# Kernel optimization log

Measured on AMD Instinct MI355X. Metric: run time of the kernel, lower is better.

## Reference

```python
import jax, jax.numpy as jnp
import numpy as np


def setup_inputs() -> dict:
    key = jax.random.key(0)
    k1, k2, k3 = jax.random.split(key, 3)
    B, Cin, H, W = 16, 128, 56, 56
    Cout, Kh, Kw = 256, 3, 3
    tensor = jax.random.normal(k1, (B, Cin, H, W), dtype=jnp.float32)
    weights = jax.random.normal(k2, (Cout, Cin, Kh, Kw), dtype=jnp.float32) * 0.05
    bias = jax.random.normal(k3, (Cout,), dtype=jnp.float32) * 0.05
    return {"tensor": tensor, "weights": weights, "bias": bias}


def reference(tensor, weights, bias):
    # OpticalConvolution: unfold (im2col) -> per-output-channel augmented dot
    # products (w . patch + b). Mathematically this is a standard 2D conv with
    # bias, expressed here as one fused conv instead of a per-channel loop.
    stride, padding, dilation = (1, 1), ((1, 1), (1, 1)), (1, 1)
    out = jax.lax.conv_general_dilated(
        tensor, weights,
        window_strides=stride,
        padding=padding,
        rhs_dilation=dilation,
        dimension_numbers=("NCHW", "OIHW", "NCHW"),
    )
    return out + bias[None, :, None, None]  # [B, Cout, H_out, W_out]
```

## Files before the change

kernel.cpp:

```cpp
#include <hip/hip_runtime.h>

typedef unsigned short ushort_t;
typedef unsigned int uint_t;

#define CIN   128
#define COUT  256
#define HH    56
#define WW    56
#define HWSZ  3136
#define BATCH 16
#define NPIX  50176
#define KTOT  1152

typedef __attribute__((ext_vector_type(8))) short bf16x8;
typedef __attribute__((ext_vector_type(4))) float f32x4;

__device__ __forceinline__ ushort_t f2bf(float v) {
    union { float f; uint_t u; } c; c.f = v;
    uint_t u = c.u;
    u += 0x7FFFu + ((u >> 16) & 1u);
    return (ushort_t)(u >> 16);
}

__global__ void wt_xform(const float* __restrict__ w, ushort_t* __restrict__ out) {
    int idx = blockIdx.x * 256 + threadIdx.x;
    int co  = idx / KTOT;
    int k   = idx - co * KTOT;
    int pos = k >> 7;
    int ci  = k & 127;
    out[idx] = f2bf(w[co * KTOT + ci * 9 + pos]);
}

__global__ void in_xform(const float* __restrict__ in, ushort_t* __restrict__ out) {
    __shared__ ushort_t tile[WW * 130];
    int by = blockIdx.x;
    int b  = by / HH;
    int y  = by - b * HH;
    const float* src = in + (size_t)b * CIN * HWSZ + (size_t)y * WW;
    for (int idx = threadIdx.x; idx < CIN * WW; idx += 256) {
        int ci = idx / WW;
        int x  = idx - ci * WW;
        tile[x * 130 + ci] = f2bf(src[(size_t)ci * HWSZ + x]);
    }
    __syncthreads();
    ushort_t* dst = out + (size_t)by * WW * CIN;
    for (int idx = threadIdx.x; idx < CIN * WW; idx += 256) {
        int x  = idx >> 7;
        int ci = idx & 127;
        dst[idx] = tile[x * 130 + ci];
    }
}

__global__ __launch_bounds__(256, 2) void conv_gemm(
    const ushort_t* __restrict__ Wt,
    const ushort_t* __restrict__ Ib,
    const float* __restrict__ bias,
    float* __restrict__ out,
    const ushort_t* __restrict__ guard)
{
    __shared__ ushort_t A_lds[128 * 32];
    __shared__ ushort_t B_lds[128 * 32];

    const int tid  = threadIdx.x;
    const int wave = tid >> 6;
    const int lane = tid & 63;
    const int quad = lane >> 4;
    const int l16  = lane & 15;

    const int bm = blockIdx.x & 1;
    const int bn = blockIdx.x >> 1;

    const int wm = (wave >> 1) * 64;
    const int wn = (wave & 1) * 64;

    const ushort_t* aBase[2];
    const ushort_t* pb0[2];
    int py[2], px[2];
    for (int q = 0; q < 2; ++q) {
        int slot = wave * 128 + q * 64 + lane;
        int r = slot >> 2, c = slot & 3;
        aBase[q] = Wt + (size_t)(bm * 128 + r) * KTOT + c * 8;
        int pix = bn * 128 + r;
        int b_  = pix / HWSZ;
        int rem = pix - b_ * HWSZ;
        int y_  = rem / WW;
        int x_  = rem - y_ * WW;
        py[q] = y_; px[q] = x_;
        pb0[q] = Ib + (size_t)pix * CIN + c * 8;
    }

    const f32x4 zero = {0.f, 0.f, 0.f, 0.f};
    f32x4 acc[4][4];
    for (int i = 0; i < 4; ++i)
        for (int j = 0; j < 4; ++j) acc[i][j] = zero;

    for (int pos = 0; pos < 9; ++pos) {
        const int dy = pos / 3 - 1;
        const int dx = pos - (pos / 3) * 3 - 1;
        const ushort_t* bp[2];
        bool okq[2];
        for (int q = 0; q < 2; ++q) {
            int yy = py[q] + dy, xx = px[q] + dx;
            okq[q] = ((uint_t)yy < (uint_t)HH) && ((uint_t)xx < (uint_t)WW);
            bp[q]  = pb0[q] + (dy * WW + dx) * CIN;
        }
        for (int cc = 0; cc < 4; ++cc) {
            for (int q = 0; q < 2; ++q) {
                __builtin_amdgcn_global_load_lds(
                    (const __attribute__((address_space(1))) void*)(aBase[q] + pos * 128 + cc * 32),
                    (__attribute__((address_space(3))) void*)(&A_lds[(wave * 128 + q * 64) * 8]),
                    16, 0, 0);
            }
            for (int q = 0; q < 2; ++q) {
                const ushort_t* g = okq[q] ? (bp[q] + cc * 32) : guard;
                __builtin_amdgcn_global_load_lds(
                    (const __attribute__((address_space(1))) void*)g,
                    (__attribute__((address_space(3))) void*)(&B_lds[(wave * 128 + q * 64) * 8]),
                    16, 0, 0);
            }
            __syncthreads();
            bf16x8 af[4], bfr[4];
            for (int i = 0; i < 4; ++i)
                af[i] = *(const bf16x8*)&A_lds[(wm + i * 16 + l16) * 32 + quad * 8];
            for (int j = 0; j < 4; ++j)
                bfr[j] = *(const bf16x8*)&B_lds[(wn + j * 16 + l16) * 32 + quad * 8];
            for (int i = 0; i < 4; ++i)
                for (int j = 0; j < 4; ++j)
                    acc[i][j] = __builtin_amdgcn_mfma_f32_16x16x32_bf16(
                        af[i], bfr[j], acc[i][j], 0, 0, 0);
            __syncthreads();
        }
    }

    int obase[4];
    for (int j = 0; j < 4; ++j) {
        int pix = bn * 128 + wn + j * 16 + l16;
        int b_  = pix / HWSZ;
        int rem = pix - b_ * HWSZ;
        obase[j] = b_ * (COUT * HWSZ) + rem;
    }
    for (int i = 0; i < 4; ++i) {
        for (int r = 0; r < 4; ++r) {
            int co = bm * 128 + wm + i * 16 + quad * 4 + r;
            float bv = bias[co];
            int coOff = co * HWSZ;
            for (int j = 0; j < 4; ++j) {
                out[(size_t)(obase[j] + coOff)] = acc[i][j][r] + bv;
            }
        }
    }
}

__global__ void naive_conv(const float* __restrict__ in, const float* __restrict__ w,
                           const float* __restrict__ bias, float* __restrict__ out, int total) {
    int idx = blockIdx.x * 256 + threadIdx.x;
    if (idx >= total) return;
    int x = idx % WW; int t = idx / WW;
    int y = t % HH; t /= HH;
    int co = t % COUT; int b = t / COUT;
    float s = bias[co];
    const float* wr = w + (size_t)co * KTOT;
    for (int ci = 0; ci < CIN; ++ci) {
        const float* ir = in + (size_t)(b * CIN + ci) * HWSZ;
        for (int kh = 0; kh < 3; ++kh) {
            int yy = y + kh - 1;
            if ((uint_t)yy >= (uint_t)HH) continue;
            for (int kw = 0; kw < 3; ++kw) {
                int xx = x + kw - 1;
                if ((uint_t)xx >= (uint_t)WW) continue;
                s += ir[yy * WW + xx] * wr[ci * 9 + kh * 3 + kw];
            }
        }
    }
    out[idx] = s;
}

extern "C" void kernel_launch(void* const* d_in, const int* in_sizes, int n_in,
                              void* d_out, int out_size, void* d_ws, size_t ws_size,
                              hipStream_t stream) {
    const float* tensor  = (const float*)d_in[0];
    const float* weights = (const float*)d_in[1];
    const float* bias    = (const float*)d_in[2];
    float* out = (float*)d_out;

    const size_t GUARD    = 1024;
    const size_t WT_BYTES = (size_t)COUT * KTOT * 2;
    const size_t IB_BYTES = (size_t)NPIX * CIN * 2;
    const size_t NEED     = GUARD + WT_BYTES + IB_BYTES;

    if (ws_size >= NEED) {
        ushort_t* guard = (ushort_t*)d_ws;
        ushort_t* Wt    = (ushort_t*)((char*)d_ws + GUARD);
        ushort_t* Ib    = (ushort_t*)((char*)d_ws + GUARD + WT_BYTES);
        hipMemsetAsync(d_ws, 0, GUARD, stream);
        wt_xform<<<(COUT * KTOT) / 256, 256, 0, stream>>>(weights, Wt);
        in_xform<<<BATCH * HH, 256, 0, stream>>>(tensor, Ib);
        conv_gemm<<<(COUT / 128) * (NPIX / 128), 256, 0, stream>>>(Wt, Ib, bias, out, guard);
    } else {
        int total = BATCH * COUT * HWSZ;
        naive_conv<<<(total + 255) / 256, 256, 0, stream>>>(tensor, weights, bias, out, total);
    }
}
```

Before: 136.6 us.

## Fuse input/weight prep into one kernel and process two K-chunks per barrier

Replaces the memset and the two separate layout/bf16 conversion kernels with a single prep kernel that uses float4 loads and vectorized LDS-transposed stores, and zeroes the guard itself. The GEMM now loads two 32-wide K chunks into a doubled LDS buffer per sync, halving the number of barriers. It also raises launch bounds to 4 blocks per CU. This cuts launch overhead and synchronization stalls, at the cost of more LDS per block and possible register pressure from the tighter occupancy hint.

After: 134.8 us. Within noise of the previous version (-1.3%).

```diff
diff --git a/kernel.cpp b/kernel.cpp
--- a/kernel.cpp
+++ b/kernel.cpp
@@ -22,44 +22,68 @@
     return (ushort_t)(u >> 16);
 }
 
-__global__ void wt_xform(const float* __restrict__ w, ushort_t* __restrict__ out) {
-    int idx = blockIdx.x * 256 + threadIdx.x;
-    int co  = idx / KTOT;
-    int k   = idx - co * KTOT;
-    int pos = k >> 7;
-    int ci  = k & 127;
-    out[idx] = f2bf(w[co * KTOT + ci * 9 + pos]);
-}
-
-__global__ void in_xform(const float* __restrict__ in, ushort_t* __restrict__ out) {
-    __shared__ ushort_t tile[WW * 130];
-    int by = blockIdx.x;
-    int b  = by / HH;
-    int y  = by - b * HH;
-    const float* src = in + (size_t)b * CIN * HWSZ + (size_t)y * WW;
-    for (int idx = threadIdx.x; idx < CIN * WW; idx += 256) {
-        int ci = idx / WW;
-        int x  = idx - ci * WW;
-        tile[x * 130 + ci] = f2bf(src[(size_t)ci * HWSZ + x]);
-    }
-    __syncthreads();
-    ushort_t* dst = out + (size_t)by * WW * CIN;
-    for (int idx = threadIdx.x; idx < CIN * WW; idx += 256) {
-        int x  = idx >> 7;
-        int ci = idx & 127;
-        dst[idx] = tile[x * 130 + ci];
-    }
-}
-
-__global__ __launch_bounds__(256, 2) void conv_gemm(
+__global__ __launch_bounds__(256) void prep(
+    const float* __restrict__ tensor, const float* __restrict__ weights,
+    ushort_t* __restrict__ Ib, ushort_t* __restrict__ Wt, ushort_t* __restrict__ guard)
+{
+    __shared__ ushort_t lds[8704];
+    const int tid = threadIdx.x;
+
+    if (blockIdx.x < 784) {
+        int t   = blockIdx.x;
+        int b   = t / 49;
+        int hwt = t - b * 49;
+        int hw0 = hwt * 64;
+        const float* src = tensor + (size_t)b * CIN * HWSZ + hw0;
+        for (int k = 0; k < 8; ++k) {
+            int f  = tid + k * 256;
+            int ci = f >> 4;
+            int ho = (f & 15) * 4;
+            float4 v = *(const float4*)(src + (size_t)ci * HWSZ + ho);
+            lds[(ho + 0) * 136 + ci] = f2bf(v.x);
+            lds[(ho + 1) * 136 + ci] = f2bf(v.y);
+            lds[(ho + 2) * 136 + ci] = f2bf(v.z);
+            lds[(ho + 3) * 136 + ci] = f2bf(v.w);
+        }
+        __syncthreads();
+        ushort_t* dst = Ib + ((size_t)b * HWSZ + hw0) * CIN;
+        for (int k = 0; k < 4; ++k) {
+            int s   = tid + k * 256;
+            int ho  = s >> 4;
+            int cio = (s & 15) * 8;
+            bf16x8 v = *(const bf16x8*)&lds[ho * 136 + cio];
+            *(bf16x8*)(dst + ho * 128 + cio) = v;
+        }
+    } else {
+        int co = blockIdx.x - 784;
+        const float* src = weights + (size_t)co * KTOT;
+        for (int k = 0; k < 5; ++k) {
+            int idx = tid + k * 256;
+            if (idx < KTOT) {
+                int ci  = idx / 9;
+                int pos = idx - ci * 9;
+                lds[pos * 128 + ci] = f2bf(src[idx]);
+            }
+        }
+        __syncthreads();
+        ushort_t* dst = Wt + (size_t)co * KTOT;
+        for (int k = 0; k < 5; ++k) {
+            int idx = tid + k * 256;
+            if (idx < KTOT) dst[idx] = lds[idx];
+        }
+        if (blockIdx.x == 784 && tid < 8) guard[tid] = 0;
+    }
+}
+
+__global__ __launch_bounds__(256, 4) void conv_gemm(
     const ushort_t* __restrict__ Wt,
     const ushort_t* __restrict__ Ib,
     const float* __restrict__ bias,
     float* __restrict__ out,
     const ushort_t* __restrict__ guard)
 {
-    __shared__ ushort_t A_lds[128 * 32];
-    __shared__ ushort_t B_lds[128 * 32];
+    __shared__ ushort_t A_lds[2 * 128 * 32];
+    __shared__ ushort_t B_lds[2 * 128 * 32];
 
     const int tid  = threadIdx.x;
     const int wave = tid >> 6;
@@ -88,6 +112,7 @@
         py[q] = y_; px[q] = x_;
         pb0[q] = Ib + (size_t)pix * CIN + c * 8;
     }
+    const int ldsOff = (wave * 128) * 8;
 
     const f32x4 zero = {0.f, 0.f, 0.f, 0.f};
     f32x4 acc[4][4];
@@ -104,30 +129,35 @@
             okq[q] = ((uint_t)yy < (uint_t)HH) && ((uint_t)xx < (uint_t)WW);
             bp[q]  = pb0[q] + (dy * WW + dx) * CIN;
         }
-        for (int cc = 0; cc < 4; ++cc) {
-            for (int q = 0; q < 2; ++q) {
-                __builtin_amdgcn_global_load_lds(
-                    (const __attribute__((address_space(1))) void*)(aBase[q] + pos * 128 + cc * 32),
-                    (__attribute__((address_space(3))) void*)(&A_lds[(wave * 128 + q * 64) * 8]),
-                    16, 0, 0);
-            }
-            for (int q = 0; q < 2; ++q) {
-                const ushort_t* g = okq[q] ? (bp[q] + cc * 32) : guard;
-                __builtin_amdgcn_global_load_lds(
-                    (const __attribute__((address_space(1))) void*)g,
-                    (__attribute__((address_space(3))) void*)(&B_lds[(wave * 128 + q * 64) * 8]),
-                    16, 0, 0);
+        for (int cc2 = 0; cc2 < 2; ++cc2) {
+            for (int p = 0; p < 2; ++p) {
+                const int cc = cc2 * 2 + p;
+                for (int q = 0; q < 2; ++q) {
+                    __builtin_amdgcn_global_load_lds(
+                        (const __attribute__((address_space(1))) void*)(aBase[q] + pos * 128 + cc * 32),
+                        (__attribute__((address_space(3))) void*)(&A_lds[p * 4096 + ldsOff + q * 512]),
+                        16, 0, 0);
+                }
+                for (int q = 0; q < 2; ++q) {
+                    const ushort_t* g = okq[q] ? (bp[q] + cc * 32) : guard;
+                    __builtin_amdgcn_global_load_lds(
+                        (const __attribute__((address_space(1))) void*)g,
+                        (__attribute__((address_space(3))) void*)(&B_lds[p * 4096 + ldsOff + q * 512]),
+                        16, 0, 0);
+                }
             }
             __syncthreads();
-            bf16x8 af[4], bfr[4];
-            for (int i = 0; i < 4; ++i)
-                af[i] = *(const bf16x8*)&A_lds[(wm + i * 16 + l16) * 32 + quad * 8];
-            for (int j = 0; j < 4; ++j)
-                bfr[j] = *(const bf16x8*)&B_lds[(wn + j * 16 + l16) * 32 + quad * 8];
-            for (int i = 0; i < 4; ++i)
+            for (int p = 0; p < 2; ++p) {
+                bf16x8 af[4], bfr[4];
+                for (int i = 0; i < 4; ++i)
+                    af[i] = *(const bf16x8*)&A_lds[p * 4096 + (wm + i * 16 + l16) * 32 + quad * 8];
                 for (int j = 0; j < 4; ++j)
-                    acc[i][j] = __builtin_amdgcn_mfma_f32_16x16x32_bf16(
-                        af[i], bfr[j], acc[i][j], 0, 0, 0);
+                    bfr[j] = *(const bf16x8*)&B_lds[p * 4096 + (wn + j * 16 + l16) * 32 + quad * 8];
+                for (int i = 0; i < 4; ++i)
+                    for (int j = 0; j < 4; ++j)
+                        acc[i][j] = __builtin_amdgcn_mfma_f32_16x16x32_bf16(
+                            af[i], bfr[j], acc[i][j], 0, 0, 0);
+            }
             __syncthreads();
         }
     }
@@ -192,9 +222,7 @@
         ushort_t* guard = (ushort_t*)d_ws;
         ushort_t* Wt    = (ushort_t*)((char*)d_ws + GUARD);
         ushort_t* Ib    = (ushort_t*)((char*)d_ws + GUARD + WT_BYTES);
-        hipMemsetAsync(d_ws, 0, GUARD, stream);
-        wt_xform<<<(COUT * KTOT) / 256, 256, 0, stream>>>(weights, Wt);
-        in_xform<<<BATCH * HH, 256, 0, stream>>>(tensor, Ib);
+        prep<<<784 + COUT, 256, 0, stream>>>(tensor, weights, Ib, Wt, guard);
         conv_gemm<<<(COUT / 128) * (NPIX / 128), 256, 0, stream>>>(Wt, Ib, bias, out, guard);
     } else {
         int total = BATCH * COUT * HWSZ;
```
